# Kernel optimization log

Hardware: AMD Instinct MI355X
Metric: run time of the kernel (lower is better)

The kernel has to match this reference:

```python
import jax, jax.numpy as jnp
import numpy as np

B, S, D = 4, 2048, 1024
H, HD = 16, 64            # num heads, head dim (H*HD == D)
FF = 4096                  # llama intermediate size
EPS = 1e-6
THETA = 10000.0


def rms_norm(x, w):
    v = jnp.mean(jnp.square(x), axis=-1, keepdims=True)
    return x * jax.lax.rsqrt(v + EPS) * w


def apply_rope(x, pos):
    # x: [B,H,S,HD]; HF llama rotate_half convention
    inv = 1.0 / (THETA ** (jnp.arange(0, HD, 2, dtype=jnp.float32) / HD))  # [HD/2]
    ang = pos[:, None].astype(jnp.float32) * inv[None, :]                   # [S,HD/2]
    cos = jnp.concatenate([jnp.cos(ang), jnp.cos(ang)], -1)[None, None]     # [1,1,S,HD]
    sin = jnp.concatenate([jnp.sin(ang), jnp.sin(ang)], -1)[None, None]
    x1, x2 = jnp.split(x, 2, axis=-1)
    return x * cos + jnp.concatenate([-x2, x1], axis=-1) * sin


def setup_inputs() -> dict:
    key = jax.random.key(0)
    ks = jax.random.split(key, 12)
    p = lambda k, shp: (0.02 * jax.random.normal(k, shp, dtype=jnp.float32))
    return {
        "chunk_hidden_states": jax.random.normal(ks[0], (B, S, D), dtype=jnp.float32),
        "Wq": p(ks[1], (D, D)),
        "Wk": p(ks[2], (D, D)),
        "Wv": p(ks[3], (D, D)),
        "Wo": p(ks[4], (D, D)),
        "ln1_w": jnp.ones((D,), dtype=jnp.float32),
        "ln2_w": jnp.ones((D,), dtype=jnp.float32),
        "Wgate": p(ks[5], (FF, D)),
        "Wup": p(ks[6], (FF, D)),
        "Wdown": p(ks[7], (D, FF)),
        "W_out": p(ks[8], (1024, D)),
        "b_out": jnp.zeros((1024,), dtype=jnp.float32),
    }


def reference(chunk_hidden_states, Wq, Wk, Wv, Wo, ln1_w, ln2_w,
              Wgate, Wup, Wdown, W_out, b_out):
    x = chunk_hidden_states                      # [B,S,D]
    pos = jnp.arange(S)

    # --- self attention block ---
    h = rms_norm(x, ln1_w)
    q = (h @ Wq.T).reshape(B, S, H, HD).transpose(0, 2, 1, 3)  # [B,H,S,HD]
    k = (h @ Wk.T).reshape(B, S, H, HD).transpose(0, 2, 1, 3)
    v = (h @ Wv.T).reshape(B, S, H, HD).transpose(0, 2, 1, 3)
    q = apply_rope(q, pos)
    k = apply_rope(k, pos)
    # attention_mask is None when the layer is called directly -> full (non-causal) attention
    scores = jnp.einsum("bhqd,bhkd->bhqk", q, k) / jnp.sqrt(jnp.float32(HD))
    attn = jax.nn.softmax(scores, axis=-1)
    ctx = jnp.einsum("bhqk,bhkd->bhqd", attn, v)             # [B,H,S,HD]
    ctx = ctx.transpose(0, 2, 1, 3).reshape(B, S, D)
    x = x + ctx @ Wo.T

    # --- MLP block (SwiGLU) ---
    h2 = rms_norm(x, ln2_w)
    mlp = (jax.nn.silu(h2 @ Wgate.T) * (h2 @ Wup.T)) @ Wdown.T
    x = x + mlp

    # --- output head ---
    logits = x @ W_out.T + b_out                 # [B,S,1024]
    return logits.reshape(-1, 8, 1024)
```

## Files before the change

### kernel.cpp

```cpp
#include <hip/hip_runtime.h>

#define TB 4
#define TS 2048
#define TD 1024
#define TH 16
#define THD 64
#define TFF 4096
#define TTOK (TB*TS)

typedef unsigned int  uint32;
typedef unsigned short u16;
typedef short s8v __attribute__((ext_vector_type(8)));
typedef short s4bf __attribute__((ext_vector_type(4)));
typedef float f4v __attribute__((ext_vector_type(4)));

#define BF16_MAGIC 0x3f803f80u

__device__ __forceinline__ u16 f2bf(float f){
    uint32 u = __float_as_uint(f);
    u += 0x7fffu + ((u >> 16) & 1u);
    return (u16)(u >> 16);
}
__device__ __forceinline__ float bf2f(u16 h){
    return __uint_as_float(((uint32)h) << 16);
}
__device__ __forceinline__ void gload_lds16(const void* g, void* l){
    __builtin_amdgcn_global_load_lds(
        (const __attribute__((address_space(1))) unsigned int*)g,
        (__attribute__((address_space(3))) unsigned int*)l,
        16, 0, 0);
}
__device__ __forceinline__ void bar(){
    asm volatile("" ::: "memory");
    __builtin_amdgcn_s_barrier();
    asm volatile("" ::: "memory");
}
#define WAITVM(N) asm volatile("s_waitcnt vmcnt(" #N ")" ::: "memory")

struct CvtDesc { const void* src; void* dst; int n; int mode; };
struct CvtArgs { CvtDesc d[13]; };

__global__ __launch_bounds__(256)
void cvt_all(CvtArgs a, const uint32* __restrict__ flag){
    const bool isbf = (*flag == BF16_MAGIC);
    CvtDesc dd = a.d[blockIdx.y];
    if (dd.mode == 2){
        float* cosT = (float*)dd.dst;
        float* sinT = cosT + TS*32;
        for (int i = blockIdx.x*256 + threadIdx.x; i < dd.n; i += 256*gridDim.x){
            int s = i >> 5, f = i & 31;
            double inv = pow(10000.0, -(double)f/32.0);
            double ang = (double)s * inv;
            cosT[i] = (float)cos(ang);
            sinT[i] = (float)sin(ang);
        }
        return;
    }
    int n4 = dd.n >> 2;
    if (dd.mode == 1){
        float* dst = (float*)dd.dst;
        for (int i = blockIdx.x*256 + threadIdx.x; i < n4; i += 256*gridDim.x){
            float4 v;
            if (isbf){
                ushort4 u = ((const ushort4*)dd.src)[i];
                v = make_float4(bf2f(u.x), bf2f(u.y), bf2f(u.z), bf2f(u.w));
            } else v = ((const float4*)dd.src)[i];
            ((float4*)dst)[i] = v;
        }
        return;
    }
    for (int i = blockIdx.x*256 + threadIdx.x; i < n4; i += 256*gridDim.x){
        ushort4 o;
        if (isbf) o = ((const ushort4*)dd.src)[i];
        else {
            float4 v = ((const float4*)dd.src)[i];
            o.x=f2bf(v.x); o.y=f2bf(v.y); o.z=f2bf(v.z); o.w=f2bf(v.w);
        }
        size_t di = i;
        if (dd.mode >= 3){
            int row = i >> 8, c4 = i & 255;
            int drow = ((row >> 6) << 7) + (row & 63) + ((dd.mode == 4) ? 64 : 0);
            di = (size_t)drow*256 + c4;
        }
        ((ushort4*)dd.dst)[di] = o;
    }
}

__global__ __launch_bounds__(256)
void rmsnorm_k(const float* __restrict__ x, const float* __restrict__ w, u16* __restrict__ out){
    int row = blockIdx.x, tid = threadIdx.x;
    float4 xv = ((const float4*)(x + (size_t)row*TD))[tid];
    float s = xv.x*xv.x + xv.y*xv.y + xv.z*xv.z + xv.w*xv.w;
    #pragma unroll
    for (int off = 32; off > 0; off >>= 1) s += __shfl_xor(s, off);
    __shared__ float red[4];
    if ((tid & 63) == 0) red[tid >> 6] = s;
    __syncthreads();
    float tot = red[0]+red[1]+red[2]+red[3];
    float rs = rsqrtf(tot * (1.0f/TD) + 1e-6f);
    float4 wv = ((const float4*)w)[tid];
    ushort4 o;
    o.x = f2bf(xv.x*rs*wv.x); o.y = f2bf(xv.y*rs*wv.y);
    o.z = f2bf(xv.z*rs*wv.z); o.w = f2bf(xv.w*rs*wv.w);
    ((ushort4*)(out + (size_t)row*TD))[tid] = o;
}

enum { EPI_ADDF32 = 1, EPI_OUT = 3, EPI_QKVROPE = 4, EPI_ADDBF16 = 5, EPI_GATEUP = 6 };

template<int EPI>
__global__ __launch_bounds__(256)
void gemm_bt(const u16* __restrict__ A, int lda,
             const u16* __restrict__ W, int ldw,
             int K,
             void* __restrict__ outp, int ldo,
             const float* __restrict__ bias,
             const uint32* __restrict__ flag,
             u16* __restrict__ q_out, u16* __restrict__ k_out, u16* __restrict__ vt_out,
             const float* __restrict__ cosT, const float* __restrict__ sinT,
             const float* __restrict__ resid)
{
    __shared__ __align__(16) u16 SMEM[2*128*64];
    u16* As = SMEM;
    u16* Bs = SMEM + 128*64;
    const int tid  = threadIdx.x;
    const int wave = tid >> 6;
    const int lane = tid & 63;
    const int nbx = gridDim.x;
    const int lin = blockIdx.y * nbx + blockIdx.x;
    const int swz = (lin & 7) * ((nbx * gridDim.y) >> 3) + (lin >> 3);
    const int tm = (swz / nbx) * 128;
    const int tn = (swz % nbx) * 128;
    const int wm = (wave >> 1) * 64;
    const int wn = (wave &  1) * 64;

    f4v acc[4][4] = {};

    const int srow8 = lane >> 3;
    const int ch    = lane & 7;
    const int lrow  = lane & 15;
    const int lq    = lane >> 4;

    const u16* Ag = A + (size_t)(tm + wave*32 + srow8)*lda + ((ch ^ srow8) << 3);
    const u16* Wg = W + (size_t)(tn + wave*32 + srow8)*ldw + ((ch ^ srow8) << 3);

    for (int k0 = 0; k0 < K; k0 += 64){
        __syncthreads();
        #pragma unroll
        for (int i8 = 0; i8 < 4; i8++){
            gload_lds16(Ag + (size_t)(i8*8)*lda + k0, As + (wave*32 + i8*8)*64);
            gload_lds16(Wg + (size_t)(i8*8)*ldw + k0, Bs + (wave*32 + i8*8)*64);
        }
        __syncthreads();

        #pragma unroll
        for (int kk = 0; kk < 2; kk++){
            s8v a[4], b[4];
            #pragma unroll
            for (int i = 0; i < 4; i++){
                int row = wm + i*16 + lrow;
                a[i] = *(const s8v*)(As + row*64 + (((kk*4 + lq) ^ (lrow & 7)) << 3));
            }
            #pragma unroll
            for (int j = 0; j < 4; j++){
                int row = wn + j*16 + lrow;
                b[j] = *(const s8v*)(Bs + row*64 + (((kk*4 + lq) ^ (lrow & 7)) << 3));
            }
            #pragma unroll
            for (int i = 0; i < 4; i++)
                #pragma unroll
                for (int j = 0; j < 4; j++)
                    acc[i][j] = __builtin_amdgcn_mfma_f32_16x16x32_bf16(a[i], b[j], acc[i][j], 0, 0, 0);
        }
    }

    if constexpr (EPI == EPI_QKVROPE){
        const int ncol0 = tn + wn;
        if (ncol0 < 2048){
            u16* dst = (ncol0 < 1024) ? q_out : k_out;
            const int cbase = ncol0 & 1023;
            #pragma unroll
            for (int i = 0; i < 4; i++){
                #pragma unroll
                for (int r = 0; r < 4; r++){
                    int row = tm + wm + i*16 + lq*4 + r;
                    int s = row & (TS-1);
                    #pragma unroll
                    for (int j = 0; j < 2; j++){
                        int d = j*16 + lrow;
                        float c  = cosT[s*32 + d];
                        float sn = sinT[s*32 + d];
                        float x1 = acc[i][j][r], x2 = acc[i][j+2][r];
                        dst[(size_t)row*TD + cbase + d]      = f2bf(x1*c - x2*sn);
                        dst[(size_t)row*TD + cbase + d + 32] = f2bf(x2*c + x1*sn);
                    }
                }
            }
        } else {
            #pragma unroll
            for (int i = 0; i < 4; i++)
                #pragma unroll
                for (int j = 0; j < 4; j++)
                    #pragma unroll
                    for (int r = 0; r < 4; r++){
                        int row = tm + wm + i*16 + lq*4 + r;
                        int col = ncol0 - 2048 + j*16 + lrow;
                        int bb = row >> 11, s = row & (TS-1);
                        int hh = col >> 6, hd = col & 63;
                        vt_out[((size_t)(bb*TH + hh)*THD + hd)*TS + s] = f2bf(acc[i][j][r]);
                    }
        }
        return;
    }

    bool obf = false;
    if (EPI == EPI_OUT) obf = (*flag == BF16_MAGIC);
    #pragma unroll
    for (int i = 0; i < 4; i++){
        #pragma unroll
        for (int j = 0; j < 4; j++){
            #pragma unroll
            for (int r = 0; r < 4; r++){
                int row = tm + wm + i*16 + lq*4 + r;
                int col = tn + wn + j*16 + lrow;
                size_t idx = (size_t)row*ldo + col;
                float val = acc[i][j][r];
                if constexpr (EPI == EPI_ADDF32){
                    float* o = (float*)outp;
                    o[idx] += val;
                } else if constexpr (EPI == EPI_ADDBF16){
                    ((u16*)outp)[idx] = f2bf(resid[idx] + val);
                } else {
                    float v2 = val + bias[col];
                    if (obf) ((u16*)outp)[idx] = f2bf(v2);
                    else     ((float*)outp)[idx] = v2;
                }
            }
        }
    }
}

template<int EPI>
__global__ __launch_bounds__(512, 2)
void gemm256(const u16* __restrict__ A, int lda,
             const u16* __restrict__ W, int ldw,
             int K,
             void* __restrict__ outp, int ldo,
             const float* __restrict__ resid)
{
    __shared__ __align__(16) u16 SM[2][2*256*64];
    const int tid  = threadIdx.x;
    const int wave = tid >> 6;
    const int lane = tid & 63;
    const int wm = wave >> 2;
    const int wn = wave & 3;
    const int lrow = lane & 15;
    const int lq   = lane >> 4;
    const int srow8 = lane >> 3;
    const int ch    = lane & 7;

    const int nbx = gridDim.x;
    const int lin = blockIdx.y * nbx + blockIdx.x;
    const int swz = (lin & 7) * ((nbx * gridDim.y) >> 3) + (lin >> 3);
    const int tm = (swz / nbx) * 256;
    const int tn = (swz % nbx) * 256;

    const int NT = K >> 6;

    const u16* Ag = A + (size_t)(tm + wave*8 + srow8)*lda + ((ch ^ srow8) << 3);
    const u16* Wg = W + (size_t)(tn + wave*8 + srow8)*ldw + ((ch ^ srow8) << 3);

    f4v acc[2][4][2][2] = {};
    s8v a[2][4];
    s8v b[2][2];

    auto stageA = [&](int bufi, int g, int t){
        size_t k0 = (size_t)t * 64;
        #pragma unroll
        for (int r = 0; r < 2; r++)
            gload_lds16(Ag + (size_t)(g*128 + r*64)*lda + k0,
                        &SM[bufi][(g*128 + r*64 + wave*8)*64]);
    };
    auto stageB = [&](int bufi, int h, int t){
        size_t k0 = (size_t)t * 64;
        #pragma unroll
        for (int r = 0; r < 2; r++)
            gload_lds16(Wg + (size_t)(h*128 + r*64)*ldw + k0,
                        &SM[bufi][256*64 + (h*128 + r*64 + wave*8)*64]);
    };
    auto ldA = [&](int bufi, int g){
        #pragma unroll
        for (int kk = 0; kk < 2; kk++)
            #pragma unroll
            for (int i = 0; i < 4; i++){
                int row = g*128 + wm*64 + i*16 + lrow;
                a[kk][i] = *(const s8v*)(&SM[bufi][row*64 + (((kk*4 + lq) ^ (lrow & 7)) << 3)]);
            }
    };
    auto ldB = [&](int bufi, int h){
        #pragma unroll
        for (int kk = 0; kk < 2; kk++)
            #pragma unroll
            for (int j = 0; j < 2; j++){
                int row = h*128 + wn*32 + j*16 + lrow;
                b[kk][j] = *(const s8v*)(&SM[bufi][256*64 + row*64 + (((kk*4 + lq) ^ (lrow & 7)) << 3)]);
            }
    };
    auto mmac = [&](int g, int h){
        __builtin_amdgcn_s_setprio(1);
        #pragma unroll
        for (int kk = 0; kk < 2; kk++)
            #pragma unroll
            for (int i = 0; i < 4; i++)
                #pragma unroll
                for (int j = 0; j < 2; j++)
                    acc[g][i][h][j] = __builtin_amdgcn_mfma_f32_16x16x32_bf16(
                        a[kk][i], b[kk][j], acc[g][i][h][j], 0, 0, 0);
        __builtin_amdgcn_s_setprio(0);
    };

    stageA(0,0,0); stageB(0,0,0); stageB(0,1,0); stageA(0,1,0);
    stageA(1,0,1); stageB(1,1,1); stageA(1,1,1);
    WAITVM(6); bar();

    for (int t = 0; t < NT-2; t++){
        const int buf = t & 1, nb = buf ^ 1;
        ldA(buf,0); ldB(buf,0);
        stageB(nb,0,t+1);
        bar(); mmac(0,0); bar();
        ldB(buf,1);
        stageA(buf,0,t+2);
        bar(); mmac(0,1); bar();
        ldA(buf,1);
        stageB(buf,1,t+2);
        bar(); mmac(1,1); bar();
        ldB(buf,0);
        stageA(buf,1,t+2);
        WAITVM(6);
        bar(); mmac(1,0); bar();
    }
    {
        const int buf = (NT-2) & 1, nb = buf ^ 1;
        ldA(buf,0); ldB(buf,0);
        stageB(nb,0,NT-1);
        bar(); mmac(0,0); bar();
        ldB(buf,1);
        bar(); mmac(0,1); bar();
        ldA(buf,1);
        bar(); mmac(1,1); bar();
        ldB(buf,0);
        WAITVM(0);
        bar(); mmac(1,0); bar();
    }
    {
        const int buf = (NT-1) & 1;
        ldA(buf,0); ldB(buf,0);
        bar(); mmac(0,0); bar();
        ldB(buf,1);
        bar(); mmac(0,1); bar();
        ldA(buf,1);
        bar(); mmac(1,1); bar();
        ldB(buf,0);
        bar(); mmac(1,0); bar();
    }

    if constexpr (EPI == EPI_GATEUP){
        bar();
        float* X = (float*)&SM[0][0];
        const int uw = wm*2 + (wn & 1);
        if (wn >= 2){
            #pragma unroll
            for (int g = 0; g < 2; g++)
            #pragma unroll
            for (int i = 0; i < 4; i++)
            #pragma unroll
            for (int h = 0; h < 2; h++)
            #pragma unroll
            for (int j = 0; j < 2; j++)
            #pragma unroll
            for (int r = 0; r < 4; r++)
                X[uw*8192 + (g*64 + i*16 + lq*4 + r)*64
                          + ((h*32 + j*16 + lrow) ^ (lq << 3))] = acc[g][i][h][j][r];
        }
        bar();
        if (wn < 2){
            u16* o = (u16*)outp;
            #pragma unroll
            for (int g = 0; g < 2; g++)
            #pragma unroll
            for (int i = 0; i < 4; i++)
            #pragma unroll
            for (int h = 0; h < 2; h++)
            #pragma unroll
            for (int j = 0; j < 2; j++)
            #pragma unroll
            for (int r = 0; r < 4; r++){
                float gv = acc[g][i][h][j][r];
                float uv = X[uw*8192 + (g*64 + i*16 + lq*4 + r)*64
                                     + ((h*32 + j*16 + lrow) ^ (lq << 3))];
                float mres = (gv / (1.0f + __expf(-gv))) * uv;
                int row = tm + g*128 + wm*64 + i*16 + lq*4 + r;
                int ff  = (tn >> 1) + h*64 + wn*32 + j*16 + lrow;
                o[(size_t)row*TFF + ff] = f2bf(mres);
            }
        }
        return;
    }

    if constexpr (EPI == EPI_ADDBF16){
        u16* o = (u16*)outp;
        #pragma unroll
        for (int g = 0; g < 2; g++)
        #pragma unroll
        for (int i = 0; i < 4; i++)
        #pragma unroll
        for (int h = 0; h < 2; h++)
        #pragma unroll
        for (int j = 0; j < 2; j++)
        #pragma unroll
        for (int r = 0; r < 4; r++){
            int row = tm + g*128 + wm*64 + i*16 + lq*4 + r;
            int col = tn + h*128 + wn*32 + j*16 + lrow;
            size_t idx = (size_t)row*ldo + col;
            o[idx] = f2bf(resid[idx] + acc[g][i][h][j][r]);
        }
        return;
    }
}

__global__ __launch_bounds__(256, 3)
void flash_attn_mfma(const u16* __restrict__ qg, const u16* __restrict__ kg,
                     const u16* __restrict__ vt, u16* __restrict__ ctx)
{
    __shared__ u16 Qs[128*64];
    __shared__ u16 Ks[2][64*64];
    __shared__ u16 VT2[2][8*64*8];
    const int tid  = threadIdx.x;
    const int wave = tid >> 6;
    const int lane = tid & 63;
    const int qd   = lane >> 4;
    const int mm   = lane & 15;
    const int lin = blockIdx.y * 16 + blockIdx.x;
    const int swz = (lin & 7) * 128 + (lin >> 3);
    const int b  = swz >> 8, h = (swz >> 4) & 15;
    const int q0 = (swz & 15) * 128;
    const size_t tok0 = (size_t)b * TS;
    const u16* vtb = vt + (size_t)(b*TH + h)*THD*TS;
    const int rl = lane >> 3, ch = lane & 7;

    auto stageKV = [&](int bufi, int kt2){
        #pragma unroll
        for (int i = 0; i < 2; i++){
            int row = wave*16 + i*8 + rl;
            const u16* gp = kg + (tok0 + kt2*64 + row)*TD + h*THD + ((ch ^ (row & 7)) << 3);
            gload_lds16(gp, Ks[bufi] + (wave*16 + i*8)*64);
        }
        #pragma unroll
        for (int ii = 0; ii < 2; ii++){
            int kb = wave*2 + ii;
            const u16* gp = vtb + (size_t)lane*TS + kt2*64 + kb*8;
            gload_lds16(gp, VT2[bufi] + kb*64*8);
        }
    };

    #pragma unroll
    for (int i = 0; i < 4; i++){
        int row = wave*32 + i*8 + rl;
        const u16* gp = qg + (tok0 + q0 + row)*TD + h*THD + ((ch ^ (row & 7)) << 3);
        gload_lds16(gp, Qs + (wave*32 + i*8)*64);
    }
    stageKV(0, 0);
    __syncthreads();

    s8v qf[2][2];
    #pragma unroll
    for (int ct = 0; ct < 2; ct++){
        int row = wave*32 + ct*16 + mm;
        #pragma unroll
        for (int hs = 0; hs < 2; hs++)
            qf[ct][hs] = *(const s8v*)(Qs + row*64 + (((hs*4 + qd) ^ (row & 7)) << 3));
    }

    f4v acc[2][4] = {};
    float mrun[2] = {-3.0e38f, -3.0e38f};
    float lrun[2] = {0.0f, 0.0f};
    const float SC2 = 0.18033688011112042f;

    for (int kt = 0; kt < TS/64; kt++){
        const int buf = kt & 1;
        if (kt < TS/64 - 1) stageKV(buf ^ 1, kt + 1);

        f4v sc[4][2] = {};
        __builtin_amdgcn_s_setprio(1);
        #pragma unroll
        for (int rt = 0; rt < 4; rt++){
            int row = rt*16 + mm;
            #pragma unroll
            for (int hs = 0; hs < 2; hs++){
                s8v kf = *(const s8v*)(Ks[buf] + row*64 + (((hs*4 + qd) ^ (row & 7)) << 3));
                #pragma unroll
                for (int ct = 0; ct < 2; ct++)
                    sc[rt][ct] = __builtin_amdgcn_mfma_f32_16x16x32_bf16(kf, qf[ct][hs], sc[rt][ct], 0, 0, 0);
            }
        }
        __builtin_amdgcn_s_setprio(0);
        union VU { s4bf h[2]; s8v v; };
        VU vf8[2][4];
        #pragma unroll
        for (int t = 0; t < 2; t++){
            int kbA = 4*t + (qd >> 1);
            #pragma unroll
            for (int n = 0; n < 4; n++){
                const u16* base = VT2[buf] + ((16*n + mm)*8) + ((qd & 1) * 4);
                vf8[t][n].h[0] = *(const s4bf*)(base + kbA*512);
                vf8[t][n].h[1] = *(const s4bf*)(base + (kbA+2)*512);
            }
        }

        #pragma unroll
        for (int ct = 0; ct < 2; ct++){
            float mx = sc[0][ct][0];
            #pragma unroll
            for (int rt = 0; rt < 4; rt++)
                #pragma unroll
                for (int r = 0; r < 4; r++)
                    mx = fmaxf(mx, sc[rt][ct][r]);
            mx = fmaxf(mx, __shfl_xor(mx, 16));
            mx = fmaxf(mx, __shfl_xor(mx, 32));
            float mn = fmaxf(mrun[ct], mx * SC2);
            float alpha = __builtin_amdgcn_exp2f(mrun[ct] - mn);
            mrun[ct] = mn;
            float ls = 0.0f;
            uint32 pk[4][2];
            #pragma unroll
            for (int rt = 0; rt < 4; rt++){
                float p0 = __builtin_amdgcn_exp2f(fmaf(sc[rt][ct][0], SC2, -mn));
                float p1 = __builtin_amdgcn_exp2f(fmaf(sc[rt][ct][1], SC2, -mn));
                float p2 = __builtin_amdgcn_exp2f(fmaf(sc[rt][ct][2], SC2, -mn));
                float p3 = __builtin_amdgcn_exp2f(fmaf(sc[rt][ct][3], SC2, -mn));
                ls += (p0 + p1) + (p2 + p3);
                pk[rt][0] = (__float_as_uint(p0) >> 16) | (__float_as_uint(p1) & 0xFFFF0000u);
                pk[rt][1] = (__float_as_uint(p2) >> 16) | (__float_as_uint(p3) & 0xFFFF0000u);
            }
            ls += __shfl_xor(ls, 16);
            ls += __shfl_xor(ls, 32);
            lrun[ct] = lrun[ct]*alpha + ls;
            #pragma unroll
            for (int r = 0; r < 4; r++){
                float ar = __shfl(alpha, (lane & 48) + qd*4 + r);
                #pragma unroll
                for (int n = 0; n < 4; n++)
                    acc[ct][n][r] *= ar;
            }
            __builtin_amdgcn_s_setprio(1);
            #pragma unroll
            for (int t = 0; t < 2; t++){
                union { uint32 u[4]; s8v s; } pu;
                pu.u[0] = pk[2*t][0];   pu.u[1] = pk[2*t][1];
                pu.u[2] = pk[2*t+1][0]; pu.u[3] = pk[2*t+1][1];
                #pragma unroll
                for (int n = 0; n < 4; n++)
                    acc[ct][n] = __builtin_amdgcn_mfma_f32_16x16x32_bf16(pu.s, vf8[t][n].v, acc[ct][n], 0, 0, 0);
            }
            __builtin_amdgcn_s_setprio(0);
        }

        if (kt < TS/64 - 1){
            WAITVM(0);
            bar();
        }
    }
    #pragma unroll
    for (int ct = 0; ct < 2; ct++){
        float rli = 1.0f / lrun[ct];
        #pragma unroll
        for (int r = 0; r < 4; r++){
            float ir = __shfl(rli, (lane & 48) + qd*4 + r);
            int row = q0 + wave*32 + ct*16 + qd*4 + r;
            u16* op = ctx + (tok0 + row)*TD + h*THD + mm;
            #pragma unroll
            for (int n = 0; n < 4; n++)
                op[16*n] = f2bf(acc[ct][n][r] * ir);
        }
    }
}

extern "C" void kernel_launch(void* const* d_in, const int* in_sizes, int n_in,
                              void* d_out, int out_size, void* d_ws, size_t ws_size,
                              hipStream_t stream)
{
    const uint32* flag = (const uint32*)d_in[5];
    char* ws = (char*)d_ws;
    size_t off = 0;
    auto alloc = [&](size_t bytes) -> void* {
        void* p = ws + off;
        off += (bytes + 255) & ~(size_t)255;
        return p;
    };
    float* xf   = (float*)alloc((size_t)TTOK*TD*4);
    u16*   hbf  = (u16*)  alloc((size_t)TTOK*TD*2);
    u16*   qb   = (u16*)  alloc((size_t)TTOK*TD*2);
    u16*   kb   = (u16*)  alloc((size_t)TTOK*TD*2);
    u16*   cb   = (u16*)  alloc((size_t)TTOK*TD*2);
    u16*   vt   = (u16*)  alloc((size_t)TTOK*TD*2);
    u16*   wqkv = (u16*)  alloc((size_t)3*TD*TD*2);
    u16*   wo   = (u16*)  alloc((size_t)TD*TD*2);
    u16*   wfu  = (u16*)  alloc((size_t)2*TFF*TD*2);
    u16*   wd   = (u16*)  alloc((size_t)TD*TFF*2);
    u16*   wou  = (u16*)  alloc((size_t)TD*TD*2);
    float* ln1  = (float*)alloc(TD*4);
    float* ln2  = (float*)alloc(TD*4);
    float* bo   = (float*)alloc(TD*4);
    float* cosT = (float*)alloc((size_t)TS*32*4*2);
    float* sinT = cosT + TS*32;
    u16*   mbuf = qb;
    (void)ws_size; (void)in_sizes; (void)n_in; (void)out_size;

    CvtArgs ca;
    ca.d[0]  = { d_in[0],  xf,            TTOK*TD, 1 };
    ca.d[1]  = { d_in[1],  wqkv,          TD*TD,   0 };
    ca.d[2]  = { d_in[2],  wqkv + (size_t)TD*TD,   TD*TD, 0 };
    ca.d[3]  = { d_in[3],  wqkv + (size_t)2*TD*TD, TD*TD, 0 };
    ca.d[4]  = { d_in[4],  wo,            TD*TD,   0 };
    ca.d[5]  = { d_in[7],  wfu,           TFF*TD,  3 };
    ca.d[6]  = { d_in[8],  wfu,           TFF*TD,  4 };
    ca.d[7]  = { d_in[9],  wd,            TD*TFF,  0 };
    ca.d[8]  = { d_in[10], wou,           TD*TD,   0 };
    ca.d[9]  = { d_in[5],  ln1,           TD,      1 };
    ca.d[10] = { d_in[6],  ln2,           TD,      1 };
    ca.d[11] = { d_in[11], bo,            TD,      1 };
    ca.d[12] = { nullptr,  cosT,          TS*32,   2 };
    cvt_all<<<dim3(256,13),256,0,stream>>>(ca, flag);

    rmsnorm_k<<<TTOK,256,0,stream>>>(xf, ln1, hbf);
    gemm_bt<EPI_QKVROPE><<<dim3(24, TTOK/128),256,0,stream>>>(
        hbf, TD, wqkv, TD, TD, nullptr, 0, nullptr, nullptr,
        qb, kb, vt, cosT, sinT, nullptr);
    flash_attn_mfma<<<dim3(TS/128, TB*TH),256,0,stream>>>(qb, kb, vt, cb);
    gemm_bt<EPI_ADDF32><<<dim3(TD/128, TTOK/128),256,0,stream>>>(
        cb, TD, wo, TD, TD, xf, TD, nullptr, nullptr,
        nullptr, nullptr, nullptr, nullptr, nullptr, nullptr);

    rmsnorm_k<<<TTOK,256,0,stream>>>(xf, ln2, hbf);
    gemm256<EPI_GATEUP><<<dim3(2*TFF/256, TTOK/256),512,0,stream>>>(
        hbf, TD, wfu, TD, TD, mbuf, TFF, nullptr);
    gemm_bt<EPI_ADDBF16><<<dim3(TD/128, TTOK/128),256,0,stream>>>(
        mbuf, TFF, wd, TFF, TFF, hbf, TD, nullptr, nullptr,
        nullptr, nullptr, nullptr, nullptr, nullptr, xf);

    gemm_bt<EPI_OUT><<<dim3(TD/128, TTOK/128),256,0,stream>>>(
        hbf, TD, wou, TD, TD, d_out, TD, bo, flag,
        nullptr, nullptr, nullptr, nullptr, nullptr, nullptr);
}
```

Baseline: 675.1 us.

## Add 256x128 tile GEMM kernel for Wo, down-proj and output projections

After: 653.3 us. 3.2% less time.

```diff
diff --git a/kernel.cpp b/kernel.cpp
--- a/kernel.cpp
+++ b/kernel.cpp
@@ -405,25 +405,145 @@
         }
         return;
     }
-
-    if constexpr (EPI == EPI_ADDBF16){
-        u16* o = (u16*)outp;
-        #pragma unroll
-        for (int g = 0; g < 2; g++)
-        #pragma unroll
-        for (int i = 0; i < 4; i++)
-        #pragma unroll
-        for (int h = 0; h < 2; h++)
-        #pragma unroll
-        for (int j = 0; j < 2; j++)
-        #pragma unroll
-        for (int r = 0; r < 4; r++){
-            int row = tm + g*128 + wm*64 + i*16 + lq*4 + r;
-            int col = tn + h*128 + wn*32 + j*16 + lrow;
-            size_t idx = (size_t)row*ldo + col;
-            o[idx] = f2bf(resid[idx] + acc[g][i][h][j][r]);
-        }
-        return;
+}
+
+template<int EPI>
+__global__ __launch_bounds__(512, 2)
+void gemm256n128(const u16* __restrict__ A, int lda,
+                 const u16* __restrict__ W, int ldw,
+                 int K,
+                 void* __restrict__ outp, int ldo,
+                 const float* __restrict__ resid,
+                 const float* __restrict__ bias,
+                 const uint32* __restrict__ flag)
+{
+    __shared__ __align__(16) u16 SM[2][(256+128)*64];
+    const int tid  = threadIdx.x;
+    const int wave = tid >> 6;
+    const int lane = tid & 63;
+    const int wm = wave >> 2;
+    const int wn = wave & 3;
+    const int lrow = lane & 15;
+    const int lq   = lane >> 4;
+    const int srow8 = lane >> 3;
+    const int ch    = lane & 7;
+
+    const int nbx = gridDim.x;
+    const int lin = blockIdx.y * nbx + blockIdx.x;
+    const int swz = (lin & 7) * ((nbx * gridDim.y) >> 3) + (lin >> 3);
+    const int tm = (swz / nbx) * 256;
+    const int tn = (swz % nbx) * 128;
+
+    const int NT = K >> 6;
+
+    const u16* Ag = A + (size_t)(tm + wave*8 + srow8)*lda + ((ch ^ srow8) << 3);
+    const u16* Wg = W + (size_t)(tn + wave*8 + srow8)*ldw + ((ch ^ srow8) << 3);
+
+    f4v acc[2][4][2] = {};
+    s8v a[2][4];
+    s8v b[2][2];
+
+    auto stageA = [&](int bufi, int g, int t){
+        size_t k0 = (size_t)t * 64;
+        #pragma unroll
+        for (int r = 0; r < 2; r++)
+            gload_lds16(Ag + (size_t)(g*128 + r*64)*lda + k0,
+                        &SM[bufi][(g*128 + r*64 + wave*8)*64]);
+    };
+    auto stageB = [&](int bufi, int t){
+        size_t k0 = (size_t)t * 64;
+        #pragma unroll
+        for (int r = 0; r < 2; r++)
+            gload_lds16(Wg + (size_t)(r*64)*ldw + k0,
+                        &SM[bufi][256*64 + (r*64 + wave*8)*64]);
+    };
+    auto ldA = [&](int bufi, int g){
+        #pragma unroll
+        for (int kk = 0; kk < 2; kk++)
+            #pragma unroll
+            for (int i = 0; i < 4; i++){
+                int row = g*128 + wm*64 + i*16 + lrow;
+                a[kk][i] = *(const s8v*)(&SM[bufi][row*64 + (((kk*4 + lq) ^ (lrow & 7)) << 3)]);
+            }
+    };
+    auto ldB = [&](int bufi){
+        #pragma unroll
+        for (int kk = 0; kk < 2; kk++)
+            #pragma unroll
+            for (int j = 0; j < 2; j++){
+                int row = wn*32 + j*16 + lrow;
+                b[kk][j] = *(const s8v*)(&SM[bufi][256*64 + row*64 + (((kk*4 + lq) ^ (lrow & 7)) << 3)]);
+            }
+    };
+    auto mmac = [&](int g){
+        __builtin_amdgcn_s_setprio(1);
+        #pragma unroll
+        for (int kk = 0; kk < 2; kk++)
+            #pragma unroll
+            for (int i = 0; i < 4; i++)
+                #pragma unroll
+                for (int j = 0; j < 2; j++)
+                    acc[g][i][j] = __builtin_amdgcn_mfma_f32_16x16x32_bf16(
+                        a[kk][i], b[kk][j], acc[g][i][j], 0, 0, 0);
+        __builtin_amdgcn_s_setprio(0);
+    };
+
+    stageA(0,0,0); stageB(0,0); stageA(0,1,0);
+    stageB(1,1);   stageA(1,0,1);
+    WAITVM(4); bar();
+
+    for (int t = 0; t < NT-2; t++){
+        const int buf = t & 1, nb = buf ^ 1;
+        ldA(buf,0); ldB(buf);
+        stageA(nb,1,t+1);
+        WAITVM(6);
+        bar(); mmac(0); bar();
+        ldA(buf,1);
+        stageB(buf,t+2); stageA(buf,0,t+2);
+        WAITVM(6);
+        bar(); mmac(1); bar();
+    }
+    {
+        const int buf = (NT-2) & 1, nb = buf ^ 1;
+        ldA(buf,0); ldB(buf);
+        stageA(nb,1,NT-1);
+        WAITVM(6);
+        bar(); mmac(0); bar();
+        ldA(buf,1);
+        WAITVM(0);
+        bar(); mmac(1); bar();
+    }
+    {
+        const int buf = (NT-1) & 1;
+        ldA(buf,0); ldB(buf);
+        bar(); mmac(0); bar();
+        ldA(buf,1);
+        bar(); mmac(1); bar();
+    }
+
+    bool obf = false;
+    if (EPI == EPI_OUT) obf = (*flag == BF16_MAGIC);
+    #pragma unroll
+    for (int g = 0; g < 2; g++)
+    #pragma unroll
+    for (int i = 0; i < 4; i++)
+    #pragma unroll
+    for (int j = 0; j < 2; j++)
+    #pragma unroll
+    for (int r = 0; r < 4; r++){
+        int row = tm + g*128 + wm*64 + i*16 + lq*4 + r;
+        int col = tn + wn*32 + j*16 + lrow;
+        size_t idx = (size_t)row*ldo + col;
+        float val = acc[g][i][j][r];
+        if constexpr (EPI == EPI_ADDF32){
+            ((float*)outp)[idx] += val;
+        } else if constexpr (EPI == EPI_ADDBF16){
+            ((u16*)outp)[idx] = f2bf(resid[idx] + val);
+        } else {
+            float v2 = val + bias[col];
+            if (obf) ((u16*)outp)[idx] = f2bf(v2);
+            else     ((float*)outp)[idx] = v2;
+        }
     }
 }
 
@@ -636,18 +756,15 @@
         hbf, TD, wqkv, TD, TD, nullptr, 0, nullptr, nullptr,
         qb, kb, vt, cosT, sinT, nullptr);
     flash_attn_mfma<<<dim3(TS/128, TB*TH),256,0,stream>>>(qb, kb, vt, cb);
-    gemm_bt<EPI_ADDF32><<<dim3(TD/128, TTOK/128),256,0,stream>>>(
-        cb, TD, wo, TD, TD, xf, TD, nullptr, nullptr,
-        nullptr, nullptr, nullptr, nullptr, nullptr, nullptr);
+    gemm256n128<EPI_ADDF32><<<dim3(TD/128, TTOK/256),512,0,stream>>>(
+        cb, TD, wo, TD, TD, xf, TD, nullptr, nullptr, nullptr);
 
     rmsnorm_k<<<TTOK,256,0,stream>>>(xf, ln2, hbf);
     gemm256<EPI_GATEUP><<<dim3(2*TFF/256, TTOK/256),512,0,stream>>>(
         hbf, TD, wfu, TD, TD, mbuf, TFF, nullptr);
-    gemm_bt<EPI_ADDBF16><<<dim3(TD/128, TTOK/128),256,0,stream>>>(
-        mbuf, TFF, wd, TFF, TFF, hbf, TD, nullptr, nullptr,
-        nullptr, nullptr, nullptr, nullptr, nullptr, xf);
-
-    gemm_bt<EPI_OUT><<<dim3(TD/128, TTOK/128),256,0,stream>>>(
-        hbf, TD, wou, TD, TD, d_out, TD, bo, flag,
-        nullptr, nullptr, nullptr, nullptr, nullptr, nullptr);
-}
+    gemm256n128<EPI_ADDBF16><<<dim3(TD/128, TTOK/256),512,0,stream>>>(
+        mbuf, TFF, wd, TFF, TFF, hbf, TD, xf, nullptr, nullptr);
+
+    gemm256n128<EPI_OUT><<<dim3(TD/128, TTOK/256),512,0,stream>>>(
+        hbf, TD, wou, TD, TD, d_out, TD, nullptr, bo, flag);
+}
```
